# Kernel optimization log

Measured on AMD Instinct MI355X. Metric: run time of the kernel, lower is better.

Reference implementation:

```python
import jax, jax.numpy as jnp
import numpy as np

N_ITERS = 8  # fixed iteration count standing in for ReduceToBason stepper


def _knn1(ref, tgt):
    # ref: (B, N, 3), tgt: (B, M, 3) -> nearest-neighbor index in tgt for each ref point
    diff = ref[..., :, None, :] - tgt[..., None, :, :]        # (B, N, M, 3)
    dist = jnp.linalg.norm(diff, axis=-1)                      # (B, N, M)
    idx = jnp.argmin(dist, axis=-1)                            # (B, N)
    mind = jnp.min(dist, axis=-1)                              # (B, N) (error, unused downstream)
    return mind, idx


def _svdtf(source, target):
    # Kabsch: rigid transform aligning source -> target. Returns R (...,3,3), t (...,3,1)
    cs = source.mean(axis=-2, keepdims=True)
    ct = target.mean(axis=-2, keepdims=True)
    s = source - cs
    t_ = target - ct
    M = jnp.einsum('...na,...nb->...ab', t_, s)                # (...,3,3)
    U, S, Vh = jnp.linalg.svd(M)
    R = U @ Vh
    # original code flips sign of R when det(R) ~ -1 (reflection case)
    mask = jnp.abs(jnp.linalg.det(R) + 1.0) < 1e-6
    R = jnp.where(mask[..., None, None], -R, R)
    t = jnp.swapaxes(ct, -1, -2) - R @ jnp.swapaxes(cs, -1, -2)  # (...,3,1)
    return R, t


def _apply(R, t, pts):
    # p' = R p + t applied to (..., N, 3)
    return pts @ jnp.swapaxes(R, -1, -2) + jnp.swapaxes(t, -1, -2)


def setup_inputs() -> dict:
    key = jax.random.key(0)
    k1, k2 = jax.random.split(key)
    source = jax.random.normal(k1, (8, 2048, 3), dtype=jnp.float32)
    target = jax.random.normal(k2, (8, 2048, 3), dtype=jnp.float32)
    return {"source": source, "target": target}


def reference(source, target):
    def body(temporal, _):
        _, idx = _knn1(temporal, target)
        gidx = jnp.broadcast_to(idx[..., None], idx.shape + (3,))
        knntarget = jnp.take_along_axis(target, gidx, axis=-2)  # matched pairs
        R, t = _svdtf(temporal, knntarget)
        return _apply(R, t, temporal), None

    temporal, _ = jax.lax.scan(body, source, None, length=N_ITERS)
    R, t = _svdtf(source, temporal)  # total transform source -> aligned
    return jnp.concatenate([R, t], axis=-1)  # (B, 3, 4) SE3 matrix form
```

## Files before the change

### kernel.cpp

```cpp
#include <hip/hip_runtime.h>

#define NB     8
#define NP     2048
#define NITER  8
#define TEAM   32
#define NWG    256
#define NT     512
#define TSTEPS 32

#define SLOTS_FLOATS (NB*2*TEAM*16)
#define REG_FBASE    SLOTS_FLOATS
#define WS_FLOATS    (REG_FBASE + 8)

__device__ __forceinline__ float    vldf(const float* p)          { return *(volatile const float*)p; }
__device__ __forceinline__ void     vstf(float* p, float v)       { *(volatile float*)p = v; }
__device__ __forceinline__ unsigned vldu(const unsigned* p)       { return *(volatile const unsigned*)p; }
__device__ __forceinline__ void     vstu(unsigned* p, unsigned v) { *(volatile unsigned*)p = v; }
__device__ __forceinline__ void     waitvm()                      { asm volatile("s_waitcnt vmcnt(0)" ::: "memory"); }

__device__ void polar3x3f(const float* Min, float* R) {
  float X[9];
  #pragma unroll
  for (int i = 0; i < 9; ++i) X[i] = Min[i];
  #pragma unroll 1
  for (int it = 0; it < 12; ++it) {
    const float C0 = X[4]*X[8]-X[5]*X[7];
    const float C1 = X[5]*X[6]-X[3]*X[8];
    const float C2 = X[3]*X[7]-X[4]*X[6];
    const float C3 = X[2]*X[7]-X[1]*X[8];
    const float C4 = X[0]*X[8]-X[2]*X[6];
    const float C5 = X[1]*X[6]-X[0]*X[7];
    const float C6 = X[1]*X[5]-X[2]*X[4];
    const float C7 = X[2]*X[3]-X[0]*X[5];
    const float C8 = X[0]*X[4]-X[1]*X[3];
    const float det = X[0]*C0 + X[1]*C1 + X[2]*C2;
    const float ad  = fabsf(det);
    const float g   = (ad > 1e-30f) ? exp2f(-0.33333333333f * log2f(ad)) : 1.0f;
    const float ds  = (ad > 1e-30f) ? det : 1e-30f;
    const float h   = 0.5f / (g * ds);
    const float gh  = 0.5f * g;
    X[0]=gh*X[0]+h*C0; X[1]=gh*X[1]+h*C1; X[2]=gh*X[2]+h*C2;
    X[3]=gh*X[3]+h*C3; X[4]=gh*X[4]+h*C4; X[5]=gh*X[5]+h*C5;
    X[6]=gh*X[6]+h*C6; X[7]=gh*X[7]+h*C7; X[8]=gh*X[8]+h*C8;
  }
  const float d = X[0]*(X[4]*X[8]-X[5]*X[7])
                + X[1]*(X[5]*X[6]-X[3]*X[8])
                + X[2]*(X[3]*X[7]-X[4]*X[6]);
  const float s = (d < 0.0f) ? -1.0f : 1.0f;
  #pragma unroll
  for (int i = 0; i < 9; ++i) R[i] = s * X[i];
}

__global__ __launch_bounds__(NT)
__attribute__((amdgpu_waves_per_eu(2, 2)))
void icp_kernel(const float* __restrict__ src, const float* __restrict__ tgt,
                float* __restrict__ out, float* __restrict__ ws)
{
  __shared__ float4 s_tgt[NP];
  __shared__ float  s_part[8][16];
  __shared__ float  s_rt[12];
  __shared__ int    s_rank;

  const int tid  = threadIdx.x;
  const int wave = tid >> 6;
  const int lane = tid & 63;

  unsigned xcc;
  asm volatile("s_getreg_b32 %0, hwreg(HW_REG_XCC_ID)" : "=s"(xcc));
  const int batch = (int)(xcc & 7u);

  if (tid == 0) {
    unsigned* reg = (unsigned*)(ws + REG_FBASE);
    const unsigned rk =
        __hip_atomic_fetch_add(&reg[batch], 1u, __ATOMIC_RELAXED, __HIP_MEMORY_SCOPE_AGENT);
    s_rank = (int)(rk & 31u);
  }

  const float* tb = tgt + (size_t)batch * NP * 3;
  for (int i = tid; i < NP; i += NT) {
    const float tx = tb[3*i+0], ty = tb[3*i+1], tz = tb[3*i+2];
    s_tgt[i] = make_float4(tx, ty, tz, 0.5f*(tx*tx + ty*ty + tz*tz));
  }
  __syncthreads();

  const int  rank = s_rank;
  const bool lead = (rank == 0);

  const int r0 = rank * 64 + wave * 8;
  const float* sb = src + (size_t)(batch * NP + r0) * 3;
  float px[8], py[8], pz[8];
  #pragma unroll
  for (int r = 0; r < 8; ++r) {
    px[r] = sb[3*r+0]; py[r] = sb[3*r+1]; pz[r] = sb[3*r+2];
  }

  float Rtot[9] = {1.f,0.f,0.f, 0.f,1.f,0.f, 0.f,0.f,1.f};
  float ttot[3] = {0.f,0.f,0.f};

  for (int round = 0; round < NITER; ++round) {
    const int      par  = round & 1;
    const unsigned want = (unsigned)(round + 1);

    float bs[8]; int bj[8];
    #pragma unroll
    for (int r = 0; r < 8; ++r) { bs[r] = 3.4e38f; bj[r] = 0; }
    #pragma unroll 4
    for (int k = 0; k < TSTEPS; ++k) {
      const int j = k * 64 + lane;
      const float4 tp = s_tgt[j];
      #pragma unroll
      for (int r = 0; r < 8; ++r) {
        const float sc = fmaf(-px[r], tp.x, fmaf(-py[r], tp.y, fmaf(-pz[r], tp.z, tp.w)));
        if (sc < bs[r]) { bs[r] = sc; bj[r] = j; }
      }
    }
    #pragma unroll
    for (int r = 0; r < 8; ++r) {
      #pragma unroll
      for (int sh = 0; sh < 6; ++sh) {
        const int   off = 32 >> sh;
        const float od  = __shfl_xor(bs[r], off);
        const int   oj  = __shfl_xor(bj[r], off);
        if (od < bs[r] || (od == bs[r] && oj < bj[r])) { bs[r] = od; bj[r] = oj; }
      }
    }

    {
      float S[15];
      #pragma unroll
      for (int i = 0; i < 15; ++i) S[i] = 0.f;
      #pragma unroll
      for (int r = 0; r < 8; ++r) {
        const float4 tm = s_tgt[bj[r]];
        S[0]+=px[r]; S[1]+=py[r]; S[2]+=pz[r];
        S[3]+=tm.x;  S[4]+=tm.y;  S[5]+=tm.z;
        S[6] +=tm.x*px[r]; S[7] +=tm.x*py[r]; S[8] +=tm.x*pz[r];
        S[9] +=tm.y*px[r]; S[10]+=tm.y*py[r]; S[11]+=tm.y*pz[r];
        S[12]+=tm.z*px[r]; S[13]+=tm.z*py[r]; S[14]+=tm.z*pz[r];
      }
      if (lane == 0) {
        #pragma unroll
        for (int i = 0; i < 15; ++i) s_part[wave][i] = S[i];
      }
    }
    __syncthreads();

    if (wave == 0) {
      const int comp = lane & 15, grp = lane >> 4;
      float v = (comp < 15) ? (s_part[2*grp][comp] + s_part[2*grp+1][comp]) : 0.f;
      v += __shfl_xor(v, 16);
      v += __shfl_xor(v, 32);

      float* slot = ws + ((((size_t)batch * 2 + par) * TEAM + rank) << 4);
      if (lane < 15) vstf(&slot[lane], v);
      waitvm();
      if (lane == 0) vstu((unsigned*)slot + 15, want);

      if ((round < NITER - 1) || lead) {
        float* sbase = ws + (((size_t)batch * 2 + par) * TEAM << 4);
        unsigned* tagq = (unsigned*)(sbase + ((size_t)lane << 4)) + 15;
        int ok, guard = 0;
        do {
          ok = (lane >= TEAM) || (vldu(tagq) == want);
          if (++guard > (1 << 15)) break;
        } while (!__all(ok));

        const float* slotq = sbase + ((size_t)lane << 4);
        float s[15];
        #pragma unroll
        for (int i = 0; i < 15; ++i)
          s[i] = (lane < TEAM) ? vldf(&slotq[i]) : 0.f;
        #pragma unroll
        for (int i = 0; i < 15; ++i) {
          s[i] += __shfl_xor(s[i], 1);
          s[i] += __shfl_xor(s[i], 2);
          s[i] += __shfl_xor(s[i], 4);
          s[i] += __shfl_xor(s[i], 8);
          s[i] += __shfl_xor(s[i], 16);
        }

        if (lane == 0) {
          const double inv = 1.0 / (double)NP;
          const double cs0=(double)s[0]*inv, cs1=(double)s[1]*inv, cs2=(double)s[2]*inv;
          const double ct0=(double)s[3]*inv, ct1=(double)s[4]*inv, ct2=(double)s[5]*inv;
          float M[9];
          M[0]=(float)((double)s[6] -(double)NP*ct0*cs0); M[1]=(float)((double)s[7] -(double)NP*ct0*cs1); M[2]=(float)((double)s[8] -(double)NP*ct0*cs2);
          M[3]=(float)((double)s[9] -(double)NP*ct1*cs0); M[4]=(float)((double)s[10]-(double)NP*ct1*cs1); M[5]=(float)((double)s[11]-(double)NP*ct1*cs2);
          M[6]=(float)((double)s[12]-(double)NP*ct2*cs0); M[7]=(float)((double)s[13]-(double)NP*ct2*cs1); M[8]=(float)((double)s[14]-(double)NP*ct2*cs2);
          float R[9]; polar3x3f(M, R);
          const float t0 = (float)(ct0 - ((double)R[0]*cs0 + (double)R[1]*cs1 + (double)R[2]*cs2));
          const float t1 = (float)(ct1 - ((double)R[3]*cs0 + (double)R[4]*cs1 + (double)R[5]*cs2));
          const float t2 = (float)(ct2 - ((double)R[6]*cs0 + (double)R[7]*cs1 + (double)R[8]*cs2));

          s_rt[0]=R[0]; s_rt[1]=R[1]; s_rt[2]=R[2];
          s_rt[3]=R[3]; s_rt[4]=R[4]; s_rt[5]=R[5];
          s_rt[6]=R[6]; s_rt[7]=R[7]; s_rt[8]=R[8];
          s_rt[9]=t0;  s_rt[10]=t1;  s_rt[11]=t2;

          if (lead) {
            float Rn[9], tn[3];
            #pragma unroll
            for (int i = 0; i < 3; ++i) {
              Rn[3*i+0] = R[3*i+0]*Rtot[0] + R[3*i+1]*Rtot[3] + R[3*i+2]*Rtot[6];
              Rn[3*i+1] = R[3*i+0]*Rtot[1] + R[3*i+1]*Rtot[4] + R[3*i+2]*Rtot[7];
              Rn[3*i+2] = R[3*i+0]*Rtot[2] + R[3*i+1]*Rtot[5] + R[3*i+2]*Rtot[8];
              tn[i]     = R[3*i+0]*ttot[0] + R[3*i+1]*ttot[1] + R[3*i+2]*ttot[2]
                        + ((i==0)?t0:(i==1)?t1:t2);
            }
            #pragma unroll
            for (int i = 0; i < 9; ++i) Rtot[i] = Rn[i];
            ttot[0]=tn[0]; ttot[1]=tn[1]; ttot[2]=tn[2];

            if (round == NITER - 1) {
              float* ob = out + batch * 12;
              ob[0]=Rtot[0]; ob[1]=Rtot[1]; ob[2] =Rtot[2]; ob[3] =ttot[0];
              ob[4]=Rtot[3]; ob[5]=Rtot[4]; ob[6] =Rtot[5]; ob[7] =ttot[1];
              ob[8]=Rtot[6]; ob[9]=Rtot[7]; ob[10]=Rtot[8]; ob[11]=ttot[2];
            }
          }
        }
      }
    }

    if (round < NITER - 1) {
      __syncthreads();
      const float R00=s_rt[0],R01=s_rt[1],R02=s_rt[2],
                  R10=s_rt[3],R11=s_rt[4],R12=s_rt[5],
                  R20=s_rt[6],R21=s_rt[7],R22=s_rt[8],
                  t0=s_rt[9], t1=s_rt[10], t2=s_rt[11];
      #pragma unroll
      for (int r = 0; r < 8; ++r) {
        const float nx = t0 + R00*px[r] + R01*py[r] + R02*pz[r];
        const float ny = t1 + R10*px[r] + R11*py[r] + R12*pz[r];
        const float nz = t2 + R20*px[r] + R21*py[r] + R22*pz[r];
        px[r]=nx; py[r]=ny; pz[r]=nz;
      }
    }
  }
}

extern "C" void kernel_launch(void* const* d_in, const int* in_sizes, int n_in,
                              void* d_out, int out_size, void* d_ws, size_t ws_size,
                              hipStream_t stream)
{
  const float* src = (const float*)d_in[0];
  const float* tgt = (const float*)d_in[1];
  float* out = (float*)d_out;
  float* ws  = (float*)d_ws;

  hipMemsetAsync(d_ws, 0, WS_FLOATS * sizeof(float), stream);

  void* args[] = { (void*)&src, (void*)&tgt, (void*)&out, (void*)&ws };
  hipLaunchCooperativeKernel(reinterpret_cast<void*>(icp_kernel),
                             dim3(NWG), dim3(NT), args, 0, stream);
}
```

Measured before the change: 151.7 us.

## Pack partial sums with per-quad tags to drop store fence and reload

Each workgroup's 15 partial sums are now written as five 16-byte stores, each holding three floats plus the round tag. This removes the vmcnt wait that separated the data writes from the flag write. Consumers poll by loading the whole 20-float slot with system-coherent dwordx4 loads and accept it once all five tags match, so the data is already in registers and no second pass of 15 volatile loads is needed. This shortens the cross-workgroup barrier on the critical path of each ICP iteration. In exchange, each poll moves more bytes, and correctness depends on 16-byte stores being atomic.

```diff
diff --git a/kernel.cpp b/kernel.cpp
--- a/kernel.cpp
+++ b/kernel.cpp
@@ -7,16 +7,29 @@
 #define NWG    256
 #define NT     512
 #define TSTEPS 32
-
-#define SLOTS_FLOATS (NB*2*TEAM*16)
+#define SLOTF  20
+
+#define SLOTS_FLOATS (NB*2*TEAM*SLOTF)
 #define REG_FBASE    SLOTS_FLOATS
 #define WS_FLOATS    (REG_FBASE + 8)
 
-__device__ __forceinline__ float    vldf(const float* p)          { return *(volatile const float*)p; }
-__device__ __forceinline__ void     vstf(float* p, float v)       { *(volatile float*)p = v; }
-__device__ __forceinline__ unsigned vldu(const unsigned* p)       { return *(volatile const unsigned*)p; }
-__device__ __forceinline__ void     vstu(unsigned* p, unsigned v) { *(volatile unsigned*)p = v; }
-__device__ __forceinline__ void     waitvm()                      { asm volatile("s_waitcnt vmcnt(0)" ::: "memory"); }
+typedef float f32x4 __attribute__((ext_vector_type(4)));
+
+__device__ __forceinline__ void st_q16(float* p, float x, float y, float z, unsigned tag) {
+  f32x4 v = { x, y, z, __uint_as_float(tag) };
+  *(volatile f32x4*)p = v;
+}
+__device__ __forceinline__ void ld_slot5(const float* p, float4& a, float4& b,
+                                         float4& c, float4& d, float4& e) {
+  asm volatile("global_load_dwordx4 %0, %5, off sc0 sc1\n\t"
+               "global_load_dwordx4 %1, %5, off offset:16 sc0 sc1\n\t"
+               "global_load_dwordx4 %2, %5, off offset:32 sc0 sc1\n\t"
+               "global_load_dwordx4 %3, %5, off offset:48 sc0 sc1\n\t"
+               "global_load_dwordx4 %4, %5, off offset:64 sc0 sc1\n\t"
+               "s_waitcnt vmcnt(0)"
+               : "=&v"(a), "=&v"(b), "=&v"(c), "=&v"(d), "=&v"(e)
+               : "v"(p) : "memory");
+}
 
 __device__ void polar3x3f(const float* Min, float* R) {
   float X[9];
@@ -151,25 +164,35 @@
       v += __shfl_xor(v, 16);
       v += __shfl_xor(v, 32);
 
-      float* slot = ws + ((((size_t)batch * 2 + par) * TEAM + rank) << 4);
-      if (lane < 15) vstf(&slot[lane], v);
-      waitvm();
-      if (lane == 0) vstu((unsigned*)slot + 15, want);
+      const int qi = (lane < 5) ? lane : 0;
+      const float qx = __shfl(v, 3*qi + 0);
+      const float qy = __shfl(v, 3*qi + 1);
+      const float qz = __shfl(v, 3*qi + 2);
+      float* slot = ws + (((size_t)batch * 2 + par) * TEAM + rank) * SLOTF;
+      if (lane < 5) {
+        st_q16(slot + 4*lane, qx, qy, qz, want);
+      }
 
       if ((round < NITER - 1) || lead) {
-        float* sbase = ws + (((size_t)batch * 2 + par) * TEAM << 4);
-        unsigned* tagq = (unsigned*)(sbase + ((size_t)lane << 4)) + 15;
+        float* sbase = ws + (((size_t)batch * 2 + par) * TEAM) * SLOTF;
+        const float* slotq = sbase + (size_t)(lane & (TEAM-1)) * SLOTF;
+        float4 a4, b4, c4, d4, e4;
         int ok, guard = 0;
         do {
-          ok = (lane >= TEAM) || (vldu(tagq) == want);
+          if (lane < TEAM) ld_slot5(slotq, a4, b4, c4, d4, e4);
+          ok = (lane >= TEAM) ||
+               (__float_as_uint(a4.w) == want && __float_as_uint(b4.w) == want &&
+                __float_as_uint(c4.w) == want && __float_as_uint(d4.w) == want &&
+                __float_as_uint(e4.w) == want);
           if (++guard > (1 << 15)) break;
         } while (!__all(ok));
 
-        const float* slotq = sbase + ((size_t)lane << 4);
-        float s[15];
-        #pragma unroll
-        for (int i = 0; i < 15; ++i)
-          s[i] = (lane < TEAM) ? vldf(&slotq[i]) : 0.f;
+        float s[15] = { a4.x,a4.y,a4.z, b4.x,b4.y,b4.z, c4.x,c4.y,c4.z,
+                        d4.x,d4.y,d4.z, e4.x,e4.y,e4.z };
+        if (lane >= TEAM) {
+          #pragma unroll
+          for (int i = 0; i < 15; ++i) s[i] = 0.f;
+        }
         #pragma unroll
         for (int i = 0; i < 15; ++i) {
           s[i] += __shfl_xor(s[i], 1);
@@ -248,9 +271,9 @@
   float* out = (float*)d_out;
   float* ws  = (float*)d_ws;
 
-  hipMemsetAsync(d_ws, 0, WS_FLOATS * sizeof(float), stream);
+  (void)hipMemsetAsync(d_ws, 0, WS_FLOATS * sizeof(float), stream);
 
   void* args[] = { (void*)&src, (void*)&tgt, (void*)&out, (void*)&ws };
-  hipLaunchCooperativeKernel(reinterpret_cast<void*>(icp_kernel),
-                             dim3(NWG), dim3(NT), args, 0, stream);
-}
+  (void)hipLaunchCooperativeKernel(reinterpret_cast<void*>(icp_kernel),
+                                   dim3(NWG), dim3(NT), args, 0, stream);
+}
```

New measurement: 142.7 us. -5.9%, faster.
